# Kernel tuning notes

Hardware: AMD Instinct MI355X
Metric: run time of the kernel (lower is better)

Reference implementation:

```python
import jax, jax.numpy as jnp
import numpy as np

BOX_WARP = 1.0
RAY_START = 2.25
RAY_END = 3.3
S = 32  # depth_resolution (coarse), N_importance = 0


def bilinear_sample(image, coords):
    """Faithful port of the custom grid_sample (align_corners=True mapping).
    image: [B, C, H, W]; coords: [B, M, 2] in [-1, 1]. Returns [B, M, C]."""
    B, C, H, W = image.shape
    ix = (coords[..., 0] + 1.0) * 0.5 * (W - 1)
    iy = (coords[..., 1] + 1.0) * 0.5 * (H - 1)
    ix0 = jnp.floor(ix)
    iy0 = jnp.floor(iy)
    ix1 = ix0 + 1.0
    iy1 = iy0 + 1.0
    # weights use UNclamped corner positions, matching the torch code
    w_nw = (ix1 - ix) * (iy1 - iy)
    w_ne = (ix - ix0) * (iy1 - iy)
    w_sw = (ix1 - ix) * (iy - iy0)
    w_se = (ix - ix0) * (iy - iy0)
    ix0c = jnp.clip(ix0, 0, W - 1).astype(jnp.int32)
    ix1c = jnp.clip(ix1, 0, W - 1).astype(jnp.int32)
    iy0c = jnp.clip(iy0, 0, H - 1).astype(jnp.int32)
    iy1c = jnp.clip(iy1, 0, H - 1).astype(jnp.int32)
    img = image.reshape(B, C, H * W)

    def gather(iyc, ixc):
        idx = iyc * W + ixc  # [B, M]
        return jnp.take_along_axis(img, idx[:, None, :], axis=2)  # [B, C, M]

    out = (gather(iy0c, ix0c) * w_nw[:, None, :]
           + gather(iy0c, ix1c) * w_ne[:, None, :]
           + gather(iy1c, ix0c) * w_sw[:, None, :]
           + gather(iy1c, ix1c) * w_se[:, None, :])
    return out.transpose(0, 2, 1)  # [B, M, C]


def setup_inputs() -> dict:
    key = jax.random.key(0)
    k1, k2, k3, k4, k5 = jax.random.split(key, 5)
    N, n_planes, C, H, W = 2, 3, 32, 256, 256
    R = 16384
    vol_planes = jax.random.normal(k1, (N, n_planes, C, H, W), dtype=jnp.float32)
    dirs = jax.random.normal(k2, (N, R, 3), dtype=jnp.float32)
    dirs = dirs / jnp.linalg.norm(dirs, axis=-1, keepdims=True)
    # camera on sphere of radius 2.7 looking through origin -> samples in box
    ray_origins = -2.7 * dirs
    w1 = jax.random.normal(k3, (C, 64), dtype=jnp.float32) * (1.0 / np.sqrt(C))
    b1 = jnp.zeros((64,), dtype=jnp.float32)
    w2 = jax.random.normal(k4, (64, 33), dtype=jnp.float32) * (1.0 / 8.0)
    b2 = jnp.zeros((33,), dtype=jnp.float32)
    return {"vol_planes": vol_planes, "ray_origins": ray_origins,
            "ray_directions": dirs, "w1": w1, "b1": b1, "w2": w2, "b2": b2}


def reference(vol_planes, ray_origins, ray_directions, w1, b1, w2, b2):
    N, n_planes, C, H, W = vol_planes.shape
    R = ray_origins.shape[1]
    # --- sample_stratified (deterministic: midpoint of each bin) ---
    t = (jnp.arange(S, dtype=vol_planes.dtype) + 0.5) / S
    d = RAY_START + (RAY_END - RAY_START) * t  # [S]
    depths = jnp.broadcast_to(d[None, None, :, None], (N, R, S, 1))
    coords = ray_origins[:, :, None, :] + depths * ray_directions[:, :, None, :]
    M = R * S
    coords = coords.reshape(N, M, 3) * (2.0 / BOX_WARP)
    # --- project_onto_planes (vol_proj=True): xyz, yzx, xzy; sampler uses xy ---
    xy = coords[..., jnp.array([0, 1])]
    yz = coords[..., jnp.array([1, 2])]
    xz = coords[..., jnp.array([0, 2])]
    proj = jnp.stack([xy, yz, xz], axis=1).reshape(N * n_planes, M, 2)
    feats = bilinear_sample(vol_planes.reshape(N * n_planes, C, H, W), proj)
    feats = feats.reshape(N, n_planes, M, C).mean(axis=1)  # aggregate planes
    # --- decoder: small MLP -> 1 sigma + 32 rgb features (EG3D style) ---
    h = jax.nn.softplus(feats @ w1 + b1)
    o = h @ w2 + b2
    sigma = o[..., :1].reshape(N, R, S, 1)
    rgb = (jax.nn.sigmoid(o[..., 1:]) * 1.002 - 0.001).reshape(N, R, S, 32)
    # --- MipRayMarcher2 ---
    deltas = depths[:, :, 1:] - depths[:, :, :-1]
    colors_mid = 0.5 * (rgb[:, :, :-1] + rgb[:, :, 1:])
    densities_mid = 0.5 * (sigma[:, :, :-1] + sigma[:, :, 1:])
    densities_mid = jax.nn.softplus(densities_mid - 1.0)
    alpha = 1.0 - jnp.exp(-deltas * densities_mid)  # [N,R,S-1,1]
    trans = jnp.cumprod(
        jnp.concatenate([jnp.ones_like(alpha[:, :, :1]), 1.0 - alpha + 1e-10],
                        axis=2), axis=2)[:, :, :-1]
    weights = alpha * trans
    rgb_final = (weights * colors_mid).sum(axis=2)  # [N, R, 32]
    return rgb_final
```

## Files before the change

kernel.cpp:

```cpp
#include <hip/hip_runtime.h>
#include <math.h>

#define HH 256
#define WW 256
#define CC 32
#define SS 32
#define NRAYS 32768
#define RPB 8
#define TEXOFF 256

#define FXB_OFF 0
#define SIG_OFF 20480
#define WST_OFF 21504
#define W2T_OFF 25600
#define ALP_OFF 31744
#define POOLSZ  32768
#define RECB_OFF 20480

typedef __attribute__((ext_vector_type(8))) short short8;
typedef __attribute__((ext_vector_type(4))) float f32x4;

__device__ __forceinline__ f32x4 mfma16(short8 a, short8 b, f32x4 c) {
    return __builtin_amdgcn_mfma_f32_16x16x32_bf16(a, b, c, 0, 0, 0);
}

__device__ __forceinline__ float bf2f(unsigned short u) {
    union { unsigned int ui; float f; } v; v.ui = ((unsigned int)u) << 16; return v.f;
}
__device__ __forceinline__ float lo2f(unsigned int w) {
    union { unsigned int ui; float f; } v; v.ui = w << 16; return v.f;
}
__device__ __forceinline__ float hi2f(unsigned int w) {
    union { unsigned int ui; float f; } v; v.ui = w & 0xffff0000u; return v.f;
}
__device__ __forceinline__ unsigned int cvtpk2(float a, float b) {
    unsigned int r;
    asm("v_cvt_pk_bf16_f32 %0, %1, %2" : "=v"(r) : "v"(a), "v"(b));
    return r;
}
__device__ __forceinline__ unsigned short f2bf_cvt(float f) {
    unsigned int r;
    asm("v_cvt_pk_bf16_f32 %0, %1, %2" : "=v"(r) : "v"(f), "v"(f));
    return (unsigned short)r;
}
__device__ __forceinline__ int iclamp(int x, int lo, int hi) {
    return x < lo ? lo : (x > hi ? hi : x);
}
__device__ __forceinline__ float softplus_f(float z) {
    return fmaxf(z, 0.f) + log1pf(expf(-fabsf(z)));
}
__device__ __forceinline__ float softplus_fast(float z) {
    return fmaxf(z, 0.f) + __logf(1.0f + __expf(-fabsf(z)));
}
__device__ __forceinline__ float sigmoid_fast(float z) {
    return __builtin_amdgcn_rcpf(1.0f + __expf(-z));
}

template<bool F32>
__device__ __forceinline__ float ldv(const void* p, size_t i) {
    if (F32) return ((const float*)p)[i];
    else     return bf2f(((const unsigned short*)p)[i]);
}

__device__ __forceinline__ int detect_f32_local(const void* __restrict__ rayo) {
    const float* f = (const float*)rayo;
    const unsigned short* u = (const unsigned short*)rayo;
    float sf = 0.f, sb = 0.f;
    #pragma unroll
    for (int i = 0; i < 8; ++i) {
        const float a = f[3 * i], b = f[3 * i + 1], c = f[3 * i + 2];
        const float nf = a * a + b * b + c * c;
        sf += fminf(fabsf(nf - 7.29f), 1e3f);
        const float x = bf2f(u[3 * i]), y = bf2f(u[3 * i + 1]), z = bf2f(u[3 * i + 2]);
        const float nb = x * x + y * y + z * z;
        sb += fminf(fabsf(nb - 7.29f), 1e3f);
    }
    return (sf < sb) ? 1 : 0;
}

__global__ __launch_bounds__(1024) void transpose_tex(
    const void* __restrict__ vol, unsigned short* __restrict__ tex,
    const void* __restrict__ rayo) {
    __shared__ __align__(16) unsigned short tb[32][129];
    __shared__ int sflag;
    const int l = threadIdx.x;
    if (l == 0) sflag = detect_f32_local(rayo);
    const int tx = l & 31, ty = l >> 5;
    const int wq = l >> 3, cq = l & 7;
    const int w0 = blockIdx.x * 128;
    const int h  = blockIdx.y;
    const int img = blockIdx.z;
    const size_t srcE = (((size_t)img * CC + ty) * HH + h) * WW + w0 + 4 * tx;
    const size_t dstE = (((size_t)img * HH + h) * WW + (w0 + wq)) * CC + 4 * cq;
    __syncthreads();
    if (sflag) {
        const float4 v = *(const float4*)((const float*)vol + srcE);
        tb[ty][4 * tx + 0] = f2bf_cvt(v.x); tb[ty][4 * tx + 1] = f2bf_cvt(v.y);
        tb[ty][4 * tx + 2] = f2bf_cvt(v.z); tb[ty][4 * tx + 3] = f2bf_cvt(v.w);
    } else {
        *(ushort4*)&tb[ty][4 * tx] = *(const ushort4*)((const unsigned short*)vol + srcE);
    }
    __syncthreads();
    ushort4 o;
    o.x = tb[4 * cq + 0][wq]; o.y = tb[4 * cq + 1][wq];
    o.z = tb[4 * cq + 2][wq]; o.w = tb[4 * cq + 3][wq];
    *(ushort4*)(tex + dstE) = o;
}

template<bool F32>
__device__ void render_mfma_body(
    const unsigned short* __restrict__ tex,
    const void* __restrict__ rayo, const void* __restrict__ rayd,
    const void* __restrict__ w1b, const void* __restrict__ b1b,
    const void* __restrict__ w2b, const void* __restrict__ b2b,
    void* __restrict__ outp, char* __restrict__ pool)
{
    const int t = threadIdx.x;
    unsigned short* fxB = (unsigned short*)(pool + FXB_OFF);
    float* sigL = (float*)(pool + SIG_OFF);
    unsigned short* w1t = (unsigned short*)(pool + WST_OFF);
    unsigned short* w2t = (unsigned short*)(pool + W2T_OFF);
    float* aL = (float*)(pool + ALP_OFF);

    for (int i = t; i < 2048; i += 256) {
        const int n = i >> 5, k = i & 31;
        w1t[i] = f2bf_cvt(ldv<F32>(w1b, (size_t)k * 64 + n));
    }
    for (int i = t; i < 3072; i += 256) {
        const int n = i >> 6, k = i & 63;
        w2t[i] = (n < 33) ? f2bf_cvt(ldv<F32>(w2b, (size_t)k * 33 + n)) : (unsigned short)0;
    }
    __syncthreads();

    const int w = t >> 6;
    const int lane = t & 63;
    const int l16 = lane & 15, quad = lane >> 4;

    short8 b1f[4];
    #pragma unroll
    for (int nt = 0; nt < 4; nt++)
        b1f[nt] = *(const short8*)(pool + WST_OFF + (nt * 16 + l16) * 64 + quad * 16);
    short8 b2f[3][2];
    #pragma unroll
    for (int nt = 0; nt < 3; nt++)
        #pragma unroll
        for (int ks = 0; ks < 2; ks++)
            b2f[nt][ks] = *(const short8*)(pool + W2T_OFF + (nt * 16 + l16) * 128 + ks * 64 + quad * 16);
    __syncthreads();

    {
        const int rl = t >> 5, s = t & 31;
        const int gray = blockIdx.x * RPB + rl;
        const size_t rb = (size_t)gray * 3;
        const float ox = ldv<F32>(rayo, rb), oy = ldv<F32>(rayo, rb + 1), oz = ldv<F32>(rayo, rb + 2);
        const float dx = ldv<F32>(rayd, rb), dy = ldv<F32>(rayd, rb + 1), dz = ldv<F32>(rayd, rb + 2);
        const float d = 2.25f + 1.05f * ((s + 0.5f) * (1.0f / 32.0f));
        const float x = (ox + d * dx) * 2.0f;
        const float y = (oy + d * dy) * 2.0f;
        const float z = (oz + d * dz) * 2.0f;
        const int j = ((t & 7) << 5) | (t >> 3);
        char* recp = pool + RECB_OFF + j * 48;
        #pragma unroll
        for (int p = 0; p < 3; p++) {
            const float u = (p == 0) ? x : ((p == 1) ? y : x);
            const float v = (p == 0) ? y : z;
            const float ixf = fmaf(u, 127.5f, 127.5f);
            const float iyf = fmaf(v, 127.5f, 127.5f);
            const float ix0f = floorf(ixf), iy0f = floorf(iyf);
            const float wx1 = ixf - ix0f, wy1 = iyf - iy0f;
            const int ix0 = iclamp((int)ix0f, 0, 255);
            const int ix1 = iclamp((int)ix0f + 1, 0, 255);
            const int iy0 = iclamp((int)iy0f, 0, 255);
            const int iy1 = iclamp((int)iy0f + 1, 0, 255);
            uint4 rec;
            rec.x = __float_as_uint(wx1);
            rec.y = __float_as_uint(wy1);
            rec.z = (unsigned int)(iy0 * WW + ix0) | ((unsigned int)(iy0 * WW + ix1) << 16);
            rec.w = (unsigned int)(iy1 * WW + ix0) | ((unsigned int)(iy1 * WW + ix1) << 16);
            *(uint4*)(recp + p * 16) = rec;
        }
    }
    __syncthreads();

    {
        const int rl = t >> 5;
        const int L  = t & 31;
        const int c4 = L & 7;
        const int sub = L >> 3;
        const int gray = blockIdx.x * RPB + rl;
        const int n = gray >> 14;
        const char* texb = (const char*)tex;
        const unsigned int cb = (unsigned int)c4 * 8;
        unsigned int pbase[3];
        #pragma unroll
        for (int p = 0; p < 3; p++)
            pbase[p] = (unsigned int)(n * 3 + p) * (HH * WW * CC * 2) + cb;
        const int g = rl * 4 + sub;
        const char* recp = pool + RECB_OFF + g * 48;

        #pragma unroll 2
        for (int k = 0; k < 8; ++k) {
            const int s = sub * 8 + k;
            float a0[4], a1[4], a2[4];
            #pragma unroll
            for (int p = 0; p < 3; p++) {
                const uint4 rc = *(const uint4*)(recp + k * 1536 + p * 16);
                const float wx1 = __uint_as_float(rc.x);
                const float wy1 = __uint_as_float(rc.y);
                const float wx0 = 1.f - wx1,  wy0 = 1.f - wy1;
                const float w00 = wx0 * wy0, w01 = wx1 * wy0, w10 = wx0 * wy1, w11 = wx1 * wy1;
                const unsigned int pb = pbase[p];
                const uint2 q00 = *(const uint2*)(texb + (pb + ((rc.z & 0xffffu) << 6)));
                const uint2 q01 = *(const uint2*)(texb + (pb + ((rc.z >> 16) << 6)));
                const uint2 q10 = *(const uint2*)(texb + (pb + ((rc.w & 0xffffu) << 6)));
                const uint2 q11 = *(const uint2*)(texb + (pb + ((rc.w >> 16) << 6)));
                const float v00[4] = { lo2f(q00.x), hi2f(q00.x), lo2f(q00.y), hi2f(q00.y) };
                const float v01[4] = { lo2f(q01.x), hi2f(q01.x), lo2f(q01.y), hi2f(q01.y) };
                const float v10[4] = { lo2f(q10.x), hi2f(q10.x), lo2f(q10.y), hi2f(q10.y) };
                const float v11[4] = { lo2f(q11.x), hi2f(q11.x), lo2f(q11.y), hi2f(q11.y) };
                #pragma unroll
                for (int i = 0; i < 4; i++) {
                    float acc = w00 * v00[i];
                    acc = fmaf(w01, v01[i], acc);
                    acc = fmaf(w10, v10[i], acc);
                    acc = fmaf(w11, v11[i], acc);
                    if (p == 0) a0[i] = acc; else if (p == 1) a1[i] = acc; else a2[i] = acc;
                }
            }
            uint2 pk;
            pk.x = cvtpk2((a0[0] + a1[0] + a2[0]) * (1.0f / 3.0f),
                          (a0[1] + a1[1] + a2[1]) * (1.0f / 3.0f));
            pk.y = cvtpk2((a0[2] + a1[2] + a2[2]) * (1.0f / 3.0f),
                          (a0[3] + a1[3] + a2[3]) * (1.0f / 3.0f));
            *(uint2*)(pool + FXB_OFF + (rl * 32 + s) * 80 + c4 * 8) = pk;
        }
    }

    float bb1[4], bb2[3];
    #pragma unroll
    for (int nt = 0; nt < 4; nt++) bb1[nt] = ldv<F32>(b1b, nt * 16 + l16);
    #pragma unroll
    for (int nt = 0; nt < 3; nt++) {
        const int n2 = nt * 16 + l16;
        bb2[nt] = (n2 < 33) ? ldv<F32>(b2b, n2) : 0.f;
    }
    __syncthreads();

    {
        char* hb = pool + WST_OFF + w * 2304;
        #pragma unroll 1
        for (int mt = 0; mt < 4; mt++) {
            const int rbase = w * 64 + mt * 16;
            const short8 a1 = *(const short8*)(pool + FXB_OFF + (rbase + l16) * 80 + quad * 16);
            #pragma unroll
            for (int nt = 0; nt < 4; nt++) {
                f32x4 hc = { bb1[nt], bb1[nt], bb1[nt], bb1[nt] };
                hc = mfma16(a1, b1f[nt], hc);
                #pragma unroll
                for (int r = 0; r < 4; r++) {
                    const float hv = softplus_fast(hc[r]);
                    *(unsigned short*)(hb + (quad * 4 + r) * 144 + (nt * 16 + l16) * 2) = f2bf_cvt(hv);
                }
            }
            const short8 a2k0 = *(const short8*)(hb + l16 * 144 + quad * 16);
            const short8 a2k1 = *(const short8*)(hb + l16 * 144 + 64 + quad * 16);
            #pragma unroll
            for (int nt = 0; nt < 3; nt++) {
                f32x4 o = { bb2[nt], bb2[nt], bb2[nt], bb2[nt] };
                o = mfma16(a2k0, b2f[nt][0], o);
                o = mfma16(a2k1, b2f[nt][1], o);
                #pragma unroll
                for (int r = 0; r < 4; r++) {
                    const int row = rbase + quad * 4 + r;
                    if (nt == 0) {
                        if (l16 == 0) sigL[row] = o[r];
                        else fxB[row * 40 + (l16 - 1)] =
                                 f2bf_cvt(fmaf(sigmoid_fast(o[r]), 1.002f, -0.001f));
                    } else if (nt == 1) {
                        fxB[row * 40 + (15 + l16)] =
                                 f2bf_cvt(fmaf(sigmoid_fast(o[r]), 1.002f, -0.001f));
                    } else if (l16 == 0) {
                        fxB[row * 40 + 31] =
                                 f2bf_cvt(fmaf(sigmoid_fast(o[r]), 1.002f, -0.001f));
                    }
                }
            }
        }
    }
    __syncthreads();

    {
        const int rl = t >> 5, sm = t & 31;
        if (sm < 31) {
            const float sp = sigL[rl * 32 + sm];
            const float sn = sigL[rl * 32 + sm + 1];
            const float m = 0.5f * (sp + sn) - 1.0f;
            const float dens = fmaxf(m, 0.f) + __logf(1.0f + __expf(-fabsf(m)));
            aL[rl * 32 + sm] = 1.0f - __expf(-(1.05f / 32.0f) * dens);
        }
    }
    __syncthreads();

    {
        const int rl = t >> 5, sm = t & 31;
        if (sm == 0) {
            float T = 1.0f;
            #pragma unroll
            for (int j = 0; j < 31; j++) {
                const float a = aL[rl * 32 + j];
                aL[rl * 32 + j] = (a * T) * 0.5f;
                T *= (1.0f - a + 1e-10f);
            }
        }
    }
    __syncthreads();

    {
        const int rl = t >> 5, c = t & 31;
        const int gr2 = blockIdx.x * RPB + rl;
        float acc = 0.0f;
        float rp = bf2f(fxB[(rl * 32 + 0) * 40 + c]);
        #pragma unroll 4
        for (int sm = 0; sm < 31; sm++) {
            const float rn = bf2f(fxB[(rl * 32 + sm + 1) * 40 + c]);
            acc = fmaf(aL[rl * 32 + sm], rp + rn, acc);
            rp = rn;
        }
        const size_t oidx = (size_t)gr2 * 32 + c;
        if (F32) ((float*)outp)[oidx] = acc;
        else     ((unsigned short*)outp)[oidx] = f2bf_cvt(acc);
    }
}

__global__ __launch_bounds__(256, 5) void render_fast(
    const unsigned short* __restrict__ tex, const void* __restrict__ rayo,
    const void* __restrict__ rayd, const void* __restrict__ w1b,
    const void* __restrict__ b1b, const void* __restrict__ w2b,
    const void* __restrict__ b2b, void* __restrict__ outp)
{
    __shared__ __align__(16) char pool[POOLSZ];
    const int t = threadIdx.x;
    if (t == 0) *(int*)pool = detect_f32_local(rayo);
    __syncthreads();
    const int f32flag = *(const int*)pool;
    if (f32flag) render_mfma_body<true >(tex, rayo, rayd, w1b, b1b, w2b, b2b, outp, pool);
    else         render_mfma_body<false>(tex, rayo, rayd, w1b, b1b, w2b, b2b, outp, pool);
}

template<bool F32>
__device__ __forceinline__ void render_body(
    const void* __restrict__ vol, const void* __restrict__ rayo,
    const void* __restrict__ rayd, const void* __restrict__ w1b,
    const void* __restrict__ b1b, const void* __restrict__ w2b,
    const void* __restrict__ b2b, void* __restrict__ outp,
    float* wsm, float (*rgbL)[SS][33], float (*sigL)[SS])
{
    const int t = threadIdx.x;
    for (int i = t; i < 4257; i += 256) {
        float v;
        if (i < 2048)       v = ldv<F32>(w1b, i);
        else if (i < 2112)  v = ldv<F32>(b1b, i - 2048);
        else if (i < 4224)  v = ldv<F32>(w2b, i - 2112);
        else                v = ldv<F32>(b2b, i - 4224);
        wsm[i] = v;
    }
    __syncthreads();

    const int rl = t >> 5;
    const int s  = t & 31;
    const int gray = blockIdx.x * RPB + rl;
    const int n = gray >> 14;

    const size_t rbase = (size_t)gray * 3;
    const float ox = ldv<F32>(rayo, rbase), oy = ldv<F32>(rayo, rbase + 1), oz = ldv<F32>(rayo, rbase + 2);
    const float dx = ldv<F32>(rayd, rbase), dy = ldv<F32>(rayd, rbase + 1), dz = ldv<F32>(rayd, rbase + 2);
    const float d = 2.25f + 1.05f * ((s + 0.5f) * (1.0f / 32.0f));
    const float x = (ox + d * dx) * 2.0f;
    const float y = (oy + d * dy) * 2.0f;
    const float z = (oz + d * dz) * 2.0f;

    float fx[32];
    #pragma unroll
    for (int c = 0; c < 32; c++) fx[c] = 0.f;

    #pragma unroll
    for (int p = 0; p < 3; p++) {
        const float u = (p == 0) ? x : ((p == 1) ? y : x);
        const float v = (p == 0) ? y : z;
        const float ixf = fmaf(u, 127.5f, 127.5f);
        const float iyf = fmaf(v, 127.5f, 127.5f);
        const float ix0f = floorf(ixf), iy0f = floorf(iyf);
        const float wx1 = ixf - ix0f, wy1 = iyf - iy0f;
        const float wx0 = 1.f - wx1,  wy0 = 1.f - wy1;
        const int ix0 = iclamp((int)ix0f, 0, 255);
        const int ix1 = iclamp((int)ix0f + 1, 0, 255);
        const int iy0 = iclamp((int)iy0f, 0, 255);
        const int iy1 = iclamp((int)iy0f + 1, 0, 255);
        const float wnw = wx0 * wy0, wne = wx1 * wy0, wsw = wx0 * wy1, wse = wx1 * wy1;
        const int i00 = iy0 * WW + ix0, i01 = iy0 * WW + ix1;
        const int i10 = iy1 * WW + ix0, i11 = iy1 * WW + ix1;
        const size_t pb = (size_t)(n * 3 + p) * CC * HH * WW;
        #pragma unroll
        for (int c = 0; c < 32; c++) {
            const size_t cb = pb + (size_t)c * (HH * WW);
            fx[c] += wnw * ldv<F32>(vol, cb + i00) + wne * ldv<F32>(vol, cb + i01)
                   + wsw * ldv<F32>(vol, cb + i10) + wse * ldv<F32>(vol, cb + i11);
        }
    }
    #pragma unroll
    for (int c = 0; c < 32; c++) fx[c] *= (1.0f / 3.0f);

    const float* W1 = wsm;
    const float* B1 = wsm + 2048;
    const float* W2 = wsm + 2112;
    const float* B2 = wsm + 4224;

    float h[64];
    #pragma unroll
    for (int j = 0; j < 64; j++) h[j] = B1[j];
    #pragma unroll
    for (int c = 0; c < 32; c++) {
        const float f = fx[c];
        #pragma unroll
        for (int j = 0; j < 64; j++) h[j] = fmaf(f, W1[c * 64 + j], h[j]);
    }
    #pragma unroll
    for (int j = 0; j < 64; j++) h[j] = softplus_f(h[j]);

    #pragma unroll 1
    for (int k = 0; k < 33; k++) {
        float zz = B2[k];
        #pragma unroll
        for (int j = 0; j < 64; j++) zz = fmaf(h[j], W2[j * 33 + k], zz);
        if (k == 0) sigL[rl][s] = zz;
        else {
            const float sg = 1.0f / (1.0f + expf(-zz));
            rgbL[rl][s][k - 1] = fmaf(sg, 1.002f, -0.001f);
        }
    }
    __syncthreads();

    const int c = t & 31;
    const float delta = 1.05f / 32.0f;
    float T = 1.0f, acc = 0.0f;
    float sig_prev = sigL[rl][0];
    float rgb_prev = rgbL[rl][0][c];
    #pragma unroll 1
    for (int sm = 0; sm < 31; sm++) {
        const float sig_next = sigL[rl][sm + 1];
        const float rgb_next = rgbL[rl][sm + 1][c];
        const float dens = softplus_f(0.5f * (sig_prev + sig_next) - 1.0f);
        const float alpha = 1.0f - expf(-delta * dens);
        acc += alpha * T * 0.5f * (rgb_prev + rgb_next);
        T *= (1.0f - alpha + 1e-10f);
        sig_prev = sig_next;
        rgb_prev = rgb_next;
    }
    const size_t oidx = (size_t)gray * 32 + c;
    if (F32) ((float*)outp)[oidx] = acc;
    else     ((unsigned short*)outp)[oidx] = f2bf_cvt(acc);
}

__global__ __launch_bounds__(256) void render_any(
    const void* __restrict__ vol, const void* __restrict__ rayo,
    const void* __restrict__ rayd, const void* __restrict__ w1b,
    const void* __restrict__ b1b, const void* __restrict__ w2b,
    const void* __restrict__ b2b, void* __restrict__ outp)
{
    __shared__ float wsm[4257];
    __shared__ float rgbL[RPB][SS][33];
    __shared__ float sigL[RPB][SS];
    __shared__ int sflag;
    if (threadIdx.x == 0) sflag = detect_f32_local(rayo);
    __syncthreads();
    const int f32flag = sflag;
    __syncthreads();
    if (f32flag) render_body<true >(vol, rayo, rayd, w1b, b1b, w2b, b2b, outp, wsm, rgbL, sigL);
    else         render_body<false>(vol, rayo, rayd, w1b, b1b, w2b, b2b, outp, wsm, rgbL, sigL);
}

extern "C" void kernel_launch(void* const* d_in, const int* in_sizes, int n_in,
                              void* d_out, int out_size, void* d_ws, size_t ws_size,
                              hipStream_t stream) {
    const void* vol  = d_in[0];
    const void* rayo = d_in[1];
    const void* rayd = d_in[2];
    const void* w1   = d_in[3];
    const void* b1   = d_in[4];
    const void* w2   = d_in[5];
    const void* b2   = d_in[6];
    unsigned short* tex = (unsigned short*)((char*)d_ws + TEXOFF);

    const size_t need = TEXOFF + (size_t)6 * HH * WW * CC * 2;

    if (ws_size >= need) {
        transpose_tex<<<dim3(WW / 128, HH, 6), dim3(1024), 0, stream>>>(vol, tex, rayo);
        render_fast<<<dim3(NRAYS / RPB), dim3(256), 0, stream>>>(
            tex, rayo, rayd, w1, b1, w2, b2, d_out);
    } else {
        render_any<<<dim3(NRAYS / RPB), dim3(256), 0, stream>>>(
            vol, rayo, rayd, w1, b1, w2, b2, d_out);
    }
}
```

Measured before the change: 232.5 us.

## Bin rays by direction and reorder render blocks for texture cache locality

```diff
diff --git a/kernel.cpp b/kernel.cpp
--- a/kernel.cpp
+++ b/kernel.cpp
@@ -9,6 +9,19 @@
 #define RPB 8
 #define TEXOFF 256
 
+#define NBINS 512
+#define NGRP 8
+#define GCAP 4608
+#define SLOTS (NGRP * GCAP)
+#define BBLOCKS (SLOTS / RPB)
+#define TEXBYTES ((size_t)6 * HH * WW * CC * 2)
+#define PERM_OFF (TEXOFF + TEXBYTES)
+#define CNT_OFF  (PERM_OFF + (size_t)SLOTS*4)
+#define RK_OFF   (CNT_OFF + (size_t)NBINS*4)
+#define BASE_OFF (RK_OFF + (size_t)NBINS*4)
+#define OK_OFF   (BASE_OFF + (size_t)NBINS*4)
+#define WS_NEED_BIN (OK_OFF + 16)
+
 #define FXB_OFF 0
 #define SIG_OFF 20480
 #define WST_OFF 21504
@@ -61,6 +74,9 @@
     if (F32) return ((const float*)p)[i];
     else     return bf2f(((const unsigned short*)p)[i]);
 }
+__device__ __forceinline__ float ldvr(const void* p, size_t i, int f32) {
+    return f32 ? ((const float*)p)[i] : bf2f(((const unsigned short*)p)[i]);
+}
 
 __device__ __forceinline__ int detect_f32_local(const void* __restrict__ rayo) {
     const float* f = (const float*)rayo;
@@ -76,6 +92,75 @@
         sb += fminf(fabsf(nb - 7.29f), 1e3f);
     }
     return (sf < sb) ? 1 : 0;
+}
+
+__device__ __forceinline__ int ray_bin(const void* __restrict__ rayd, int r, int f32) {
+    const size_t rb = (size_t)r * 3;
+    float dx = ldvr(rayd, rb, f32);
+    float dy = ldvr(rayd, rb + 1, f32);
+    const float dz = ldvr(rayd, rb + 2, f32);
+    if (dz < 0.f) { dx = -dx; dy = -dy; }
+    const int qx = iclamp((int)fmaf(dx, 8.0f, 8.0f), 0, 15);
+    const int qy = iclamp((int)fmaf(dy, 8.0f, 8.0f), 0, 15);
+    return ((r >> 14) << 8) | (qx << 4) | qy;
+}
+
+__global__ __launch_bounds__(1024) void zero_init(unsigned int* __restrict__ perm,
+                                                  int* __restrict__ cntrk) {
+    const int g = blockIdx.x * 1024 + threadIdx.x;
+    perm[g] = 0xFFFFFFFFu;
+    if (blockIdx.x == 0 && threadIdx.x < 2 * NBINS) cntrk[threadIdx.x] = 0;
+}
+
+__global__ __launch_bounds__(256) void bin_count(
+    const void* __restrict__ rayd, const void* __restrict__ rayo,
+    int* __restrict__ cnt) {
+    __shared__ int fl;
+    if (threadIdx.x == 0) fl = detect_f32_local(rayo);
+    __syncthreads();
+    const int r = blockIdx.x * 256 + threadIdx.x;
+    atomicAdd(&cnt[ray_bin(rayd, r, fl)], 1);
+}
+
+__global__ __launch_bounds__(256) void scan_bins(
+    const int* __restrict__ cnt, int* __restrict__ base, int* __restrict__ okf) {
+    __shared__ int c[NBINS];
+    __shared__ int gs[NGRP];
+    const int t = threadIdx.x;
+    c[t] = cnt[t]; c[t + 256] = cnt[t + 256];
+    __syncthreads();
+    if (t < NGRP) {
+        int acc = 0;
+        for (int i = 0; i < 64; i++) { base[t * 64 + i] = acc; acc += c[t * 64 + i]; }
+        gs[t] = acc;
+    }
+    __syncthreads();
+    if (t == 0) {
+        int ok = 1;
+        for (int g = 0; g < NGRP; g++) ok &= (gs[g] <= GCAP);
+        *okf = ok;
+    }
+}
+
+__global__ __launch_bounds__(256) void scatter_rays(
+    const void* __restrict__ rayd, const void* __restrict__ rayo,
+    const int* __restrict__ base, int* __restrict__ rk,
+    const int* __restrict__ okf, unsigned int* __restrict__ perm) {
+    __shared__ int fl;
+    if (threadIdx.x == 0) fl = detect_f32_local(rayo);
+    __syncthreads();
+    const int r = blockIdx.x * 256 + threadIdx.x;
+    unsigned int g, k;
+    if (*okf) {
+        const int b = ray_bin(rayd, r, fl);
+        g = (unsigned int)b >> 6;
+        k = (unsigned int)(base[b] + atomicAdd(&rk[b], 1));
+    } else {
+        g = (unsigned int)r >> 12;
+        k = (unsigned int)r & 4095u;
+    }
+    const unsigned int pos = ((k >> 3) << 6) | (g << 3) | (k & 7u);
+    perm[pos] = (unsigned int)r;
 }
 
 __global__ __launch_bounds__(1024) void transpose_tex(
@@ -113,7 +198,8 @@
     const void* __restrict__ rayo, const void* __restrict__ rayd,
     const void* __restrict__ w1b, const void* __restrict__ b1b,
     const void* __restrict__ w2b, const void* __restrict__ b2b,
-    void* __restrict__ outp, char* __restrict__ pool)
+    void* __restrict__ outp, char* __restrict__ pool,
+    const int gray, const int valid)
 {
     const int t = threadIdx.x;
     unsigned short* fxB = (unsigned short*)(pool + FXB_OFF);
@@ -149,8 +235,7 @@
     __syncthreads();
 
     {
-        const int rl = t >> 5, s = t & 31;
-        const int gray = blockIdx.x * RPB + rl;
+        const int s = t & 31;
         const size_t rb = (size_t)gray * 3;
         const float ox = ldv<F32>(rayo, rb), oy = ldv<F32>(rayo, rb + 1), oz = ldv<F32>(rayo, rb + 2);
         const float dx = ldv<F32>(rayd, rb), dy = ldv<F32>(rayd, rb + 1), dz = ldv<F32>(rayd, rb + 2);
@@ -187,7 +272,6 @@
         const int L  = t & 31;
         const int c4 = L & 7;
         const int sub = L >> 3;
-        const int gray = blockIdx.x * RPB + rl;
         const int n = gray >> 14;
         const char* texb = (const char*)tex;
         const unsigned int cb = (unsigned int)c4 * 8;
@@ -317,7 +401,6 @@
 
     {
         const int rl = t >> 5, c = t & 31;
-        const int gr2 = blockIdx.x * RPB + rl;
         float acc = 0.0f;
         float rp = bf2f(fxB[(rl * 32 + 0) * 40 + c]);
         #pragma unroll 4
@@ -326,9 +409,11 @@
             acc = fmaf(aL[rl * 32 + sm], rp + rn, acc);
             rp = rn;
         }
-        const size_t oidx = (size_t)gr2 * 32 + c;
-        if (F32) ((float*)outp)[oidx] = acc;
-        else     ((unsigned short*)outp)[oidx] = f2bf_cvt(acc);
+        if (valid) {
+            const size_t oidx = (size_t)gray * 32 + c;
+            if (F32) ((float*)outp)[oidx] = acc;
+            else     ((unsigned short*)outp)[oidx] = f2bf_cvt(acc);
+        }
     }
 }
 
@@ -336,15 +421,21 @@
     const unsigned short* __restrict__ tex, const void* __restrict__ rayo,
     const void* __restrict__ rayd, const void* __restrict__ w1b,
     const void* __restrict__ b1b, const void* __restrict__ w2b,
-    const void* __restrict__ b2b, void* __restrict__ outp)
+    const void* __restrict__ b2b, void* __restrict__ outp,
+    const unsigned int* __restrict__ perm)
 {
     __shared__ __align__(16) char pool[POOLSZ];
     const int t = threadIdx.x;
+    const int slot = blockIdx.x * RPB + (t >> 5);
+    const unsigned int raw = perm ? perm[slot] : (unsigned int)slot;
+    const int valid = raw < NRAYS;
+    if (!__syncthreads_or(valid)) return;
+    const int gray = valid ? (int)raw : 0;
     if (t == 0) *(int*)pool = detect_f32_local(rayo);
     __syncthreads();
     const int f32flag = *(const int*)pool;
-    if (f32flag) render_mfma_body<true >(tex, rayo, rayd, w1b, b1b, w2b, b2b, outp, pool);
-    else         render_mfma_body<false>(tex, rayo, rayd, w1b, b1b, w2b, b2b, outp, pool);
+    if (f32flag) render_mfma_body<true >(tex, rayo, rayd, w1b, b1b, w2b, b2b, outp, pool, gray, valid);
+    else         render_mfma_body<false>(tex, rayo, rayd, w1b, b1b, w2b, b2b, outp, pool, gray, valid);
 }
 
 template<bool F32>
@@ -491,12 +582,25 @@
     const void* b2   = d_in[6];
     unsigned short* tex = (unsigned short*)((char*)d_ws + TEXOFF);
 
-    const size_t need = TEXOFF + (size_t)6 * HH * WW * CC * 2;
-
-    if (ws_size >= need) {
+    const size_t need = TEXOFF + TEXBYTES;
+
+    if (ws_size >= WS_NEED_BIN) {
+        unsigned int* perm = (unsigned int*)((char*)d_ws + PERM_OFF);
+        int* cnt  = (int*)((char*)d_ws + CNT_OFF);
+        int* rk   = (int*)((char*)d_ws + RK_OFF);
+        int* base = (int*)((char*)d_ws + BASE_OFF);
+        int* okf  = (int*)((char*)d_ws + OK_OFF);
+        zero_init<<<dim3(SLOTS / 1024), dim3(1024), 0, stream>>>(perm, cnt);
+        bin_count<<<dim3(NRAYS / 256), dim3(256), 0, stream>>>(rayd, rayo, cnt);
+        scan_bins<<<dim3(1), dim3(256), 0, stream>>>(cnt, base, okf);
+        scatter_rays<<<dim3(NRAYS / 256), dim3(256), 0, stream>>>(rayd, rayo, base, rk, okf, perm);
+        transpose_tex<<<dim3(WW / 128, HH, 6), dim3(1024), 0, stream>>>(vol, tex, rayo);
+        render_fast<<<dim3(BBLOCKS), dim3(256), 0, stream>>>(
+            tex, rayo, rayd, w1, b1, w2, b2, d_out, perm);
+    } else if (ws_size >= need) {
         transpose_tex<<<dim3(WW / 128, HH, 6), dim3(1024), 0, stream>>>(vol, tex, rayo);
         render_fast<<<dim3(NRAYS / RPB), dim3(256), 0, stream>>>(
-            tex, rayo, rayd, w1, b1, w2, b2, d_out);
+            tex, rayo, rayd, w1, b1, w2, b2, d_out, nullptr);
     } else {
         render_any<<<dim3(NRAYS / RPB), dim3(256), 0, stream>>>(
             vol, rayo, rayd, w1, b1, w2, b2, d_out);
```

Measured after the change: 260.5 us. +12.0%, slower.
